# Kernel optimization log

Measured on AMD Instinct MI355X. Metric: run time of the kernel, lower is better.

Reference implementation:

```python
import jax, jax.numpy as jnp
import numpy as np

BN_EPS = 1e-5
EPS_GIN = 0.0  # pyg GINConv default eps

N_NODES = 50000
N_EDGES = 800000
D_IN = 128
D_OUT = 128


def setup_inputs() -> dict:
    key = jax.random.key(0)
    ks = jax.random.split(key, 6)
    x = jax.random.normal(ks[0], (N_NODES, D_IN), dtype=jnp.float32)
    edge_index = jax.random.randint(ks[1], (2, N_EDGES), 0, N_NODES, dtype=jnp.int32)
    # glorot-ish scale for the two Linear layers
    s1 = 1.0 / np.sqrt(D_IN)
    s2 = 1.0 / np.sqrt(D_OUT)
    W1 = jax.random.normal(ks[2], (D_IN, D_OUT), dtype=jnp.float32) * s1
    b1 = jnp.zeros((D_OUT,), dtype=jnp.float32)
    gamma = jnp.ones((D_OUT,), dtype=jnp.float32)
    beta = jnp.zeros((D_OUT,), dtype=jnp.float32)
    W2 = jax.random.normal(ks[3], (D_OUT, D_OUT), dtype=jnp.float32) * s2
    b2 = jnp.zeros((D_OUT,), dtype=jnp.float32)
    return {"x": x, "edge_index": edge_index, "W1": W1, "b1": b1,
            "gamma": gamma, "beta": beta, "W2": W2, "b2": b2}


def reference(x, edge_index, W1, b1, gamma, beta, W2, b2):
    n = x.shape[0]
    src, dst = edge_index[0], edge_index[1]  # source_to_target flow
    # scatter-add neighbor aggregation: agg[i] = sum_{(j->i)} x[j]
    agg = jax.ops.segment_sum(x[src], dst, num_segments=n)
    h = (1.0 + EPS_GIN) * x + agg  # GIN combine
    # Linear -> BatchNorm1d (training-mode batch stats, biased var) -> ReLU -> Linear
    h = h @ W1 + b1
    mean = jnp.mean(h, axis=0)
    var = jnp.var(h, axis=0)
    h = (h - mean) * jax.lax.rsqrt(var + BN_EPS) * gamma + beta
    h = jax.nn.relu(h)
    return h @ W2 + b2
```

## Files before the change

### kernel.cpp

```cpp
#include <hip/hip_runtime.h>
#include <hip/hip_bf16.h>

#define D 128
#define ELLW 64
#define BCAP 8192

typedef short bf16x8 __attribute__((ext_vector_type(8)));
typedef float f32x4 __attribute__((ext_vector_type(4)));

__device__ __forceinline__ ushort f32_to_bf16_rne(float f) {
    uint b = __float_as_uint(f);
    b += 0x7fffu + ((b >> 16) & 1u);
    return (ushort)(b >> 16);
}
__device__ __forceinline__ float bf16_bits_to_f32(ushort u) {
    return __uint_as_float(((uint)u) << 16);
}
__device__ __forceinline__ float blo(uint u) { return __uint_as_float(u << 16); }
__device__ __forceinline__ float bhi(uint u) { return __uint_as_float(u & 0xffff0000u); }


__global__ __launch_bounds__(512) void zero_kernel(int* __restrict__ p) {
    p[threadIdx.x] = 0;
}


__global__ __launch_bounds__(1024) void prep_scatter_kernel(const float2* __restrict__ x2,
                                                            const float* __restrict__ W1,
                                                            const float* __restrict__ W2,
                                                            const int* __restrict__ src,
                                                            const int* __restrict__ dst,
                                                            uint* __restrict__ xb,
                                                            ushort* __restrict__ W1T,
                                                            ushort* __restrict__ W2T,
                                                            uint* __restrict__ part,
                                                            int* __restrict__ bcnt,
                                                            int nhalf, int m, int nbx) {
    int b = blockIdx.x, t = threadIdx.x;
    if (b < nbx) {
        int i = b * 1024 + t;
        if (i < nhalf) {
            float2 v = x2[i];
            xb[i] = ((uint)f32_to_bf16_rne(v.y) << 16) | (uint)f32_to_bf16_rne(v.x);
        }
        return;
    }
    if (b < nbx + 32) {
        int wb = b - nbx;
        const float* W = (wb < 16) ? W1 : W2;
        ushort* WT = (wb < 16) ? W1T : W2T;
        int q = wb & 15;
        int nrow = q * 8 + (t >> 7);
        int k = t & 127;
        WT[nrow * D + k] = f32_to_bf16_rne(W[k * D + nrow]);
        return;
    }
    __shared__ int hist[256];
    __shared__ int cur[256];
    if (t < 256) hist[t] = 0;
    __syncthreads();

    int base = (b - nbx - 32) * 4096;
    uint v[4];
    int bk[4];
    bool ok[4];
#pragma unroll
    for (int j = 0; j < 4; ++j) {
        int e = base + j * 1024 + t;
        ok[j] = e < m;
        bk[j] = 0;
        if (ok[j]) {
            int s_ = src[e], d_ = dst[e];
            v[j] = ((uint)s_ << 16) | (uint)d_;
            bk[j] = d_ >> 8;
            atomicAdd(&hist[bk[j]], 1);
        }
    }
    __syncthreads();
    if (t < 256) {
        int h = hist[t];
        int g = h ? atomicAdd(&bcnt[t], h) : 0;
        cur[t] = t * BCAP + g;
    }
    __syncthreads();
#pragma unroll
    for (int j = 0; j < 4; ++j) {
        if (ok[j]) {
            int pos = atomicAdd(&cur[bk[j]], 1);
            if (pos - bk[j] * BCAP < BCAP)
                part[pos] = v[j];
        }
    }
}


__global__ __launch_bounds__(1024) void agg_gemm1_kernel(const uint* __restrict__ xb,
                                                         const uint* __restrict__ part,
                                                         const int* __restrict__ bcnt,
                                                         const ushort* __restrict__ W1T,
                                                         const float* __restrict__ bias,
                                                         ushort* __restrict__ h1b,
                                                         float* __restrict__ bn_sums,
                                                         int n) {
    __shared__ __align__(16) ushort hs[64 * D];
    __shared__ ushort lell[64 * ELLW];
    __shared__ int lcur[64];
    __shared__ float bs[D];
    __shared__ float bnl[2 * D];

    int tid = threadIdx.x;
    int row0 = blockIdx.x * 64;
    int bkt = row0 >> 8;
    if (tid < 64) lcur[tid] = 0;
    if (tid >= 128 && tid < 256) bs[tid - 128] = bias[tid - 128];
    if (tid >= 256 && tid < 512) bnl[tid - 256] = 0.f;
    __syncthreads();

    int cnt = min(bcnt[bkt], BCAP);
    const uint* pp = part + (size_t)bkt * BCAP;
    for (int i = tid; i < cnt; i += 1024) {
        uint v = pp[i];
        uint r2 = (v & 0xffffu) - (uint)row0;
        if (r2 < 64u) {
            int s = atomicAdd(&lcur[(int)r2], 1);
            s = min(s, ELLW - 1);
            lell[(int)r2 * ELLW + s] = (ushort)(v >> 16);
        }
    }
    __syncthreads();

    int w = tid >> 6, lane = tid & 63;
    char* hsb = (char*)hs;
    for (int i = 0; i < 4; ++i) {
        int r = w * 4 + i;
        int node = row0 + r;
        float sx = 0.f, sy = 0.f;
        if (node < n) {
            uint a = xb[node * 64 + lane];
            sx = blo(a);
            sy = bhi(a);
            int deg = min(lcur[r], ELLW);
            const ushort* lst = &lell[r * ELLW];
            int e = 0;
            for (; e + 7 < deg; e += 8) {
                uint u[8];
#pragma unroll
                for (int j = 0; j < 8; ++j) u[j] = xb[(int)lst[e + j] * 64 + lane];
#pragma unroll
                for (int j = 0; j < 8; ++j) { sx += blo(u[j]); sy += bhi(u[j]); }
            }
            if (e + 3 < deg) {
                uint u[4];
#pragma unroll
                for (int j = 0; j < 4; ++j) u[j] = xb[(int)lst[e + j] * 64 + lane];
#pragma unroll
                for (int j = 0; j < 4; ++j) { sx += blo(u[j]); sy += bhi(u[j]); }
                e += 4;
            }
            for (; e < deg; ++e) {
                uint u = xb[(int)lst[e] * 64 + lane];
                sx += blo(u);
                sy += bhi(u);
            }
        }
        uint o = ((uint)f32_to_bf16_rne(sy) << 16) | (uint)f32_to_bf16_rne(sx);
        *(uint*)(hsb + r * 256 + ((((lane >> 2) << 4) ^ ((r & 7) << 4)) | ((lane & 3) << 2))) = o;
    }
    __syncthreads();

    int band = w & 3, cq = w >> 2;
    int lrow = lane & 15, lk = lane >> 4;

    f32x4 acc[2];
#pragma unroll
    for (int f = 0; f < 2; ++f) acc[f] = (f32x4){0.f, 0.f, 0.f, 0.f};

    bf16x8 afr[4];
    int arow = band * 16 + lrow;
#pragma unroll
    for (int t = 0; t < 4; ++t)
        afr[t] = *(const bf16x8*)(hsb + arow * 256 + ((t * 64 + lk * 16) ^ ((arow & 7) << 4)));

#pragma unroll
    for (int f = 0; f < 2; ++f) {
        int nc = cq * 32 + f * 16 + lrow;
#pragma unroll
        for (int t = 0; t < 4; ++t) {
            bf16x8 bfr = *(const bf16x8*)(W1T + nc * D + t * 32 + lk * 8);
            acc[f] = __builtin_amdgcn_mfma_f32_16x16x32_bf16(afr[t], bfr, acc[f], 0, 0, 0);
        }
    }

    int rbase = row0 + band * 16 + lk * 4;
#pragma unroll
    for (int f = 0; f < 2; ++f) {
        int colc = cq * 32 + f * 16 + lrow;
        float bv = bs[colc];
        float s = 0.f, q = 0.f;
#pragma unroll
        for (int r = 0; r < 4; ++r) {
            int gr = rbase + r;
            if (gr < n) {
                float v = acc[f][r] + bv;
                h1b[(size_t)gr * D + colc] = f32_to_bf16_rne(v);
                s += v;
                q += v * v;
            }
        }
        s += __shfl_xor(s, 16, 64);
        s += __shfl_xor(s, 32, 64);
        q += __shfl_xor(q, 16, 64);
        q += __shfl_xor(q, 32, 64);
        if (lane < 16) {
            atomicAdd(&bnl[colc], s);
            atomicAdd(&bnl[D + colc], q);
        }
    }
    __syncthreads();
    if (tid < 2 * D) atomicAdd(&bn_sums[tid], bnl[tid]);
}


__global__ __launch_bounds__(256) void gemm2_kernel(const ushort* __restrict__ inb,
                                                    const ushort* __restrict__ WT,
                                                    const float* __restrict__ bias,
                                                    float* __restrict__ outp,
                                                    const float* __restrict__ gamma,
                                                    const float* __restrict__ beta,
                                                    const float* __restrict__ bn_sums,
                                                    float invn, int N) {
    __shared__ __align__(16) ushort hs[64 * D];
    __shared__ __align__(16) ushort wt[D * D];
    __shared__ float ss[2 * D];
    __shared__ float bs[D];

    int tid = threadIdx.x;
    int row0 = blockIdx.x * 64;
    if (tid < D) bs[tid] = bias[tid];
    if (tid < D) {
        float mean = bn_sums[tid] * invn;
        float var = bn_sums[D + tid] * invn - mean * mean;
        float sc = gamma[tid] * rsqrtf(var + 1e-5f);
        ss[tid] = sc;
        ss[D + tid] = beta[tid] - mean * sc;
    }
    __syncthreads();

    char* hsb = (char*)hs;
    char* wtb = (char*)wt;

#pragma unroll
    for (int it = 0; it < 8; ++it) {
        int c = it * 256 + tid;
        int wn = c >> 4, k8 = c & 15;
        bf16x8 v = *(const bf16x8*)(WT + wn * D + k8 * 8);
        *(bf16x8*)(wtb + wn * 256 + ((k8 * 16) ^ ((wn & 7) << 4))) = v;
    }
#pragma unroll
    for (int it = 0; it < 4; ++it) {
        int c = it * 256 + tid;
        int row = c >> 4, k8 = c & 15;
        int gr = row0 + row;
        bf16x8 v;
        if (gr < N) {
            v = *(const bf16x8*)(inb + (size_t)gr * D + k8 * 8);
        } else {
#pragma unroll
            for (int j = 0; j < 8; ++j) v[j] = 0;
        }
#pragma unroll
        for (int j = 0; j < 8; ++j) {
            int k = k8 * 8 + j;
            float f = bf16_bits_to_f32((ushort)v[j]);
            f = fmaxf(f * ss[k] + ss[D + k], 0.f);
            v[j] = (short)f32_to_bf16_rne(f);
        }
        *(bf16x8*)(hsb + row * 256 + ((k8 * 16) ^ ((row & 7) << 4))) = v;
    }
    __syncthreads();

    int w = tid >> 6, l = tid & 63;
    int lrow = l & 15, lk = l >> 4;

    f32x4 acc[8];
#pragma unroll
    for (int f = 0; f < 8; ++f) acc[f] = (f32x4){0.f, 0.f, 0.f, 0.f};

    bf16x8 afr[4];
    int arow = w * 16 + lrow;
#pragma unroll
    for (int t = 0; t < 4; ++t)
        afr[t] = *(const bf16x8*)(hsb + arow * 256 + ((t * 64 + lk * 16) ^ ((arow & 7) << 4)));

#pragma unroll
    for (int f = 0; f < 8; ++f) {
        int nc = f * 16 + lrow;
#pragma unroll
        for (int t = 0; t < 4; ++t) {
            bf16x8 bfr = *(const bf16x8*)(wtb + nc * 256 + ((t * 64 + lk * 16) ^ ((nc & 7) << 4)));
            acc[f] = __builtin_amdgcn_mfma_f32_16x16x32_bf16(afr[t], bfr, acc[f], 0, 0, 0);
        }
    }

    int rbase = row0 + w * 16 + lk * 4;
#pragma unroll
    for (int f = 0; f < 8; ++f) {
        int colc = f * 16 + lrow;
        float bv = bs[colc];
#pragma unroll
        for (int r = 0; r < 4; ++r) {
            int gr = rbase + r;
            if (gr < N) outp[(size_t)gr * D + colc] = acc[f][r] + bv;
        }
    }
}


extern "C" void kernel_launch(void* const* d_in, const int* in_sizes, int n_in,
                              void* d_out, int out_size, void* d_ws, size_t ws_size,
                              hipStream_t stream) {
    const float* x = (const float*)d_in[0];
    const int* edge = (const int*)d_in[1];
    const float* W1 = (const float*)d_in[2];
    const float* b1 = (const float*)d_in[3];
    const float* gamma = (const float*)d_in[4];
    const float* beta = (const float*)d_in[5];
    const float* W2 = (const float*)d_in[6];
    const float* b2 = (const float*)d_in[7];

    int n = in_sizes[0] / D;
    int m = in_sizes[1] / 2;
    const int* src = edge;
    const int* dst = edge + m;

    int nbuck = (n + 255) >> 8;

    uint* xb = (uint*)d_out;

    auto al = [](size_t o) { return (o + 63) & ~(size_t)63; };
    char* ws = (char*)d_ws;
    size_t off = 0;
    ushort* h1b = (ushort*)(ws + off); off = al(off + (size_t)n * D * sizeof(ushort));
    uint* part = (uint*)(ws + off);    off = al(off + (size_t)nbuck * BCAP * sizeof(uint));
    int* bcnt = (int*)(ws + off);      off += 256 * sizeof(int);
    float* bn_sums = (float*)(ws + off); off = al(off + 2 * D * sizeof(float));
    ushort* W1T = (ushort*)(ws + off); off = al(off + (size_t)D * D * sizeof(ushort));
    ushort* W2T = (ushort*)(ws + off); off = al(off + (size_t)D * D * sizeof(ushort));

    int nbx = (n * 64 + 1023) / 1024;
    int nbs = (m + 4095) / 4096;
    int nbg = (n + 63) / 64;

    zero_kernel<<<1, 512, 0, stream>>>(bcnt);
    prep_scatter_kernel<<<nbx + 32 + nbs, 1024, 0, stream>>>((const float2*)x, W1, W2, src, dst,
                                                             xb, W1T, W2T, part, bcnt, n * 64, m, nbx);
    agg_gemm1_kernel<<<nbg, 1024, 0, stream>>>(xb, part, bcnt, W1T, b1, h1b, bn_sums, n);
    gemm2_kernel<<<nbg, 256, 0, stream>>>(h1b, W2T, b2, (float*)d_out, gamma, beta,
                                          bn_sums, 1.0f / (float)n, n);
}
```

Measured before the change: 98.40 us.

## Fuse aggregation, GEMM1, BatchNorm and GEMM2 into persistent kernel with grid barrier

The separate agg_gemm1 and gemm2 kernels become one persistent kernel of 500 blocks, each handling up to two 64-row tiles. The GEMM1 accumulators stay in registers across a global atomic-counter barrier that waits for the BatchNorm sums to finish. After the barrier each block normalizes, applies ReLU and runs GEMM2 directly. This removes the bf16 h1 round trip through global memory and one kernel launch. The cost is a spin barrier that relies on all 500 blocks being co-resident, and fewer, more serialized blocks during the gather phase.

After: 382.8 us. 3.89x slower.

```diff
diff --git a/kernel.cpp b/kernel.cpp
--- a/kernel.cpp
+++ b/kernel.cpp
@@ -4,6 +4,7 @@
 #define D 128
 #define ELLW 64
 #define BCAP 8192
+#define GRID_FUSED 500
 
 typedef short bf16x8 __attribute__((ext_vector_type(8)));
 typedef float f32x4 __attribute__((ext_vector_type(4)));
@@ -13,14 +14,11 @@
     b += 0x7fffu + ((b >> 16) & 1u);
     return (ushort)(b >> 16);
 }
-__device__ __forceinline__ float bf16_bits_to_f32(ushort u) {
-    return __uint_as_float(((uint)u) << 16);
-}
 __device__ __forceinline__ float blo(uint u) { return __uint_as_float(u << 16); }
 __device__ __forceinline__ float bhi(uint u) { return __uint_as_float(u & 0xffff0000u); }
 
 
-__global__ __launch_bounds__(512) void zero_kernel(int* __restrict__ p) {
+__global__ __launch_bounds__(768) void zero_kernel(int* __restrict__ p) {
     p[threadIdx.x] = 0;
 }
 
@@ -94,223 +92,210 @@
 }
 
 
-__global__ __launch_bounds__(1024) void agg_gemm1_kernel(const uint* __restrict__ xb,
-                                                         const uint* __restrict__ part,
-                                                         const int* __restrict__ bcnt,
-                                                         const ushort* __restrict__ W1T,
-                                                         const float* __restrict__ bias,
-                                                         ushort* __restrict__ h1b,
-                                                         float* __restrict__ bn_sums,
-                                                         int n) {
+__global__ __launch_bounds__(1024, 8) void agg_mlp_kernel(const uint* __restrict__ xb,
+                                                          const uint* __restrict__ part,
+                                                          const int* __restrict__ bcnt,
+                                                          const ushort* __restrict__ W1T,
+                                                          const ushort* __restrict__ W2T,
+                                                          const float* __restrict__ b1,
+                                                          const float* __restrict__ b2,
+                                                          const float* __restrict__ gamma,
+                                                          const float* __restrict__ beta,
+                                                          float* __restrict__ bn_sums,
+                                                          int* __restrict__ counter,
+                                                          float* __restrict__ outp,
+                                                          float invn, int n, int nbg) {
     __shared__ __align__(16) ushort hs[64 * D];
     __shared__ ushort lell[64 * ELLW];
     __shared__ int lcur[64];
-    __shared__ float bs[D];
+    __shared__ float bs1[D], bs2[D];
     __shared__ float bnl[2 * D];
+    __shared__ float ss[2 * D];
 
     int tid = threadIdx.x;
-    int row0 = blockIdx.x * 64;
-    int bkt = row0 >> 8;
-    if (tid < 64) lcur[tid] = 0;
-    if (tid >= 128 && tid < 256) bs[tid - 128] = bias[tid - 128];
-    if (tid >= 256 && tid < 512) bnl[tid - 256] = 0.f;
-    __syncthreads();
-
-    int cnt = min(bcnt[bkt], BCAP);
-    const uint* pp = part + (size_t)bkt * BCAP;
-    for (int i = tid; i < cnt; i += 1024) {
-        uint v = pp[i];
-        uint r2 = (v & 0xffffu) - (uint)row0;
-        if (r2 < 64u) {
-            int s = atomicAdd(&lcur[(int)r2], 1);
-            s = min(s, ELLW - 1);
-            lell[(int)r2 * ELLW + s] = (ushort)(v >> 16);
-        }
-    }
-    __syncthreads();
-
     int w = tid >> 6, lane = tid & 63;
-    char* hsb = (char*)hs;
-    for (int i = 0; i < 4; ++i) {
-        int r = w * 4 + i;
-        int node = row0 + r;
-        float sx = 0.f, sy = 0.f;
-        if (node < n) {
-            uint a = xb[node * 64 + lane];
-            sx = blo(a);
-            sy = bhi(a);
-            int deg = min(lcur[r], ELLW);
-            const ushort* lst = &lell[r * ELLW];
-            int e = 0;
-            for (; e + 7 < deg; e += 8) {
-                uint u[8];
-#pragma unroll
-                for (int j = 0; j < 8; ++j) u[j] = xb[(int)lst[e + j] * 64 + lane];
-#pragma unroll
-                for (int j = 0; j < 8; ++j) { sx += blo(u[j]); sy += bhi(u[j]); }
-            }
-            if (e + 3 < deg) {
-                uint u[4];
-#pragma unroll
-                for (int j = 0; j < 4; ++j) u[j] = xb[(int)lst[e + j] * 64 + lane];
-#pragma unroll
-                for (int j = 0; j < 4; ++j) { sx += blo(u[j]); sy += bhi(u[j]); }
-                e += 4;
-            }
-            for (; e < deg; ++e) {
-                uint u = xb[(int)lst[e] * 64 + lane];
-                sx += blo(u);
-                sy += bhi(u);
-            }
-        }
-        uint o = ((uint)f32_to_bf16_rne(sy) << 16) | (uint)f32_to_bf16_rne(sx);
-        *(uint*)(hsb + r * 256 + ((((lane >> 2) << 4) ^ ((r & 7) << 4)) | ((lane & 3) << 2))) = o;
-    }
-    __syncthreads();
-
     int band = w & 3, cq = w >> 2;
     int lrow = lane & 15, lk = lane >> 4;
-
-    f32x4 acc[2];
-#pragma unroll
-    for (int f = 0; f < 2; ++f) acc[f] = (f32x4){0.f, 0.f, 0.f, 0.f};
-
-    bf16x8 afr[4];
-    int arow = band * 16 + lrow;
-#pragma unroll
-    for (int t = 0; t < 4; ++t)
-        afr[t] = *(const bf16x8*)(hsb + arow * 256 + ((t * 64 + lk * 16) ^ ((arow & 7) << 4)));
-
-#pragma unroll
-    for (int f = 0; f < 2; ++f) {
-        int nc = cq * 32 + f * 16 + lrow;
-#pragma unroll
-        for (int t = 0; t < 4; ++t) {
-            bf16x8 bfr = *(const bf16x8*)(W1T + nc * D + t * 32 + lk * 8);
-            acc[f] = __builtin_amdgcn_mfma_f32_16x16x32_bf16(afr[t], bfr, acc[f], 0, 0, 0);
-        }
-    }
-
-    int rbase = row0 + band * 16 + lk * 4;
-#pragma unroll
-    for (int f = 0; f < 2; ++f) {
-        int colc = cq * 32 + f * 16 + lrow;
-        float bv = bs[colc];
-        float s = 0.f, q = 0.f;
-#pragma unroll
-        for (int r = 0; r < 4; ++r) {
-            int gr = rbase + r;
-            if (gr < n) {
-                float v = acc[f][r] + bv;
-                h1b[(size_t)gr * D + colc] = f32_to_bf16_rne(v);
-                s += v;
-                q += v * v;
-            }
-        }
-        s += __shfl_xor(s, 16, 64);
-        s += __shfl_xor(s, 32, 64);
-        q += __shfl_xor(q, 16, 64);
-        q += __shfl_xor(q, 32, 64);
-        if (lane < 16) {
-            atomicAdd(&bnl[colc], s);
-            atomicAdd(&bnl[D + colc], q);
-        }
-    }
+    char* hsb = (char*)hs;
+
+    if (tid < D) bs1[tid] = b1[tid];
+    else if (tid < 2 * D) bs2[tid - D] = b2[tid - D];
+    if (tid >= 512 && tid < 768) bnl[tid - 512] = 0.f;
+
+    f32x4 acc[2][2];
+#pragma unroll
+    for (int s = 0; s < 2; ++s)
+#pragma unroll
+        for (int f = 0; f < 2; ++f) acc[s][f] = (f32x4){0.f, 0.f, 0.f, 0.f};
+
+#pragma unroll
+    for (int s = 0; s < 2; ++s) {
+        int tile = blockIdx.x + s * GRID_FUSED;
+        if (tile < nbg) {
+            int row0 = tile * 64;
+            int bkt = row0 >> 8;
+            __syncthreads();
+            if (tid < 64) lcur[tid] = 0;
+            __syncthreads();
+            int cnt = min(bcnt[bkt], BCAP);
+            const uint* pp = part + (size_t)bkt * BCAP;
+            for (int i = tid; i < cnt; i += 1024) {
+                uint v = pp[i];
+                uint r2 = (v & 0xffffu) - (uint)row0;
+                if (r2 < 64u) {
+                    int sl = atomicAdd(&lcur[(int)r2], 1);
+                    sl = min(sl, ELLW - 1);
+                    lell[(int)r2 * ELLW + sl] = (ushort)(v >> 16);
+                }
+            }
+            __syncthreads();
+            for (int i = 0; i < 4; ++i) {
+                int r = w * 4 + i;
+                int node = row0 + r;
+                float sx = 0.f, sy = 0.f;
+                if (node < n) {
+                    uint a = xb[node * 64 + lane];
+                    sx = blo(a);
+                    sy = bhi(a);
+                    int deg = min(lcur[r], ELLW);
+                    const ushort* lst = &lell[r * ELLW];
+                    int e = 0;
+                    for (; e + 7 < deg; e += 8) {
+                        uint u[8];
+#pragma unroll
+                        for (int j = 0; j < 8; ++j) u[j] = xb[(int)lst[e + j] * 64 + lane];
+#pragma unroll
+                        for (int j = 0; j < 8; ++j) { sx += blo(u[j]); sy += bhi(u[j]); }
+                    }
+                    if (e + 3 < deg) {
+                        uint u[4];
+#pragma unroll
+                        for (int j = 0; j < 4; ++j) u[j] = xb[(int)lst[e + j] * 64 + lane];
+#pragma unroll
+                        for (int j = 0; j < 4; ++j) { sx += blo(u[j]); sy += bhi(u[j]); }
+                        e += 4;
+                    }
+                    for (; e < deg; ++e) {
+                        uint u = xb[(int)lst[e] * 64 + lane];
+                        sx += blo(u);
+                        sy += bhi(u);
+                    }
+                }
+                uint o = ((uint)f32_to_bf16_rne(sy) << 16) | (uint)f32_to_bf16_rne(sx);
+                *(uint*)(hsb + r * 256 +
+                         ((((lane >> 2) << 4) ^ ((r & 7) << 4)) | ((lane & 3) << 2))) = o;
+            }
+            __syncthreads();
+            bf16x8 afr[4];
+            int arow = band * 16 + lrow;
+#pragma unroll
+            for (int t = 0; t < 4; ++t)
+                afr[t] = *(const bf16x8*)(hsb + arow * 256 +
+                                          ((t * 64 + lk * 16) ^ ((arow & 7) << 4)));
+#pragma unroll
+            for (int f = 0; f < 2; ++f) {
+                int nc = cq * 32 + f * 16 + lrow;
+#pragma unroll
+                for (int t = 0; t < 4; ++t) {
+                    bf16x8 bfr = *(const bf16x8*)(W1T + nc * D + t * 32 + lk * 8);
+                    acc[s][f] = __builtin_amdgcn_mfma_f32_16x16x32_bf16(afr[t], bfr, acc[s][f], 0, 0, 0);
+                }
+            }
+            int rbase = row0 + band * 16 + lk * 4;
+#pragma unroll
+            for (int f = 0; f < 2; ++f) {
+                int colc = cq * 32 + f * 16 + lrow;
+                float bv = bs1[colc];
+                float s1 = 0.f, q1 = 0.f;
+#pragma unroll
+                for (int r = 0; r < 4; ++r) {
+                    float v = acc[s][f][r] + bv;
+                    acc[s][f][r] = v;
+                    int gr = rbase + r;
+                    if (gr < n) { s1 += v; q1 += v * v; }
+                }
+                s1 += __shfl_xor(s1, 16, 64);
+                s1 += __shfl_xor(s1, 32, 64);
+                q1 += __shfl_xor(q1, 16, 64);
+                q1 += __shfl_xor(q1, 32, 64);
+                if (lane < 16) {
+                    atomicAdd(&bnl[colc], s1);
+                    atomicAdd(&bnl[D + colc], q1);
+                }
+            }
+        }
+    }
+
     __syncthreads();
     if (tid < 2 * D) atomicAdd(&bn_sums[tid], bnl[tid]);
-}
-
-
-__global__ __launch_bounds__(256) void gemm2_kernel(const ushort* __restrict__ inb,
-                                                    const ushort* __restrict__ WT,
-                                                    const float* __restrict__ bias,
-                                                    float* __restrict__ outp,
-                                                    const float* __restrict__ gamma,
-                                                    const float* __restrict__ beta,
-                                                    const float* __restrict__ bn_sums,
-                                                    float invn, int N) {
-    __shared__ __align__(16) ushort hs[64 * D];
-    __shared__ __align__(16) ushort wt[D * D];
-    __shared__ float ss[2 * D];
-    __shared__ float bs[D];
-
-    int tid = threadIdx.x;
-    int row0 = blockIdx.x * 64;
-    if (tid < D) bs[tid] = bias[tid];
+    __threadfence();
+    __syncthreads();
+    if (tid == 0) {
+        atomicAdd(counter, 1);
+        while (atomicAdd(counter, 0) < GRID_FUSED) __builtin_amdgcn_s_sleep(2);
+    }
+    __syncthreads();
+    __threadfence();
+
+    if (tid < 2 * D) ss[tid] = atomicAdd(&bn_sums[tid], 0.0f);
+    __syncthreads();
     if (tid < D) {
-        float mean = bn_sums[tid] * invn;
-        float var = bn_sums[D + tid] * invn - mean * mean;
+        float mean = ss[tid] * invn;
+        float var = ss[D + tid] * invn - mean * mean;
         float sc = gamma[tid] * rsqrtf(var + 1e-5f);
         ss[tid] = sc;
         ss[D + tid] = beta[tid] - mean * sc;
     }
     __syncthreads();
 
-    char* hsb = (char*)hs;
-    char* wtb = (char*)wt;
-
-#pragma unroll
-    for (int it = 0; it < 8; ++it) {
-        int c = it * 256 + tid;
-        int wn = c >> 4, k8 = c & 15;
-        bf16x8 v = *(const bf16x8*)(WT + wn * D + k8 * 8);
-        *(bf16x8*)(wtb + wn * 256 + ((k8 * 16) ^ ((wn & 7) << 4))) = v;
-    }
-#pragma unroll
-    for (int it = 0; it < 4; ++it) {
-        int c = it * 256 + tid;
-        int row = c >> 4, k8 = c & 15;
-        int gr = row0 + row;
-        bf16x8 v;
-        if (gr < N) {
-            v = *(const bf16x8*)(inb + (size_t)gr * D + k8 * 8);
-        } else {
-#pragma unroll
-            for (int j = 0; j < 8; ++j) v[j] = 0;
-        }
-#pragma unroll
-        for (int j = 0; j < 8; ++j) {
-            int k = k8 * 8 + j;
-            float f = bf16_bits_to_f32((ushort)v[j]);
-            f = fmaxf(f * ss[k] + ss[D + k], 0.f);
-            v[j] = (short)f32_to_bf16_rne(f);
-        }
-        *(bf16x8*)(hsb + row * 256 + ((k8 * 16) ^ ((row & 7) << 4))) = v;
-    }
-    __syncthreads();
-
-    int w = tid >> 6, l = tid & 63;
-    int lrow = l & 15, lk = l >> 4;
-
-    f32x4 acc[8];
-#pragma unroll
-    for (int f = 0; f < 8; ++f) acc[f] = (f32x4){0.f, 0.f, 0.f, 0.f};
-
-    bf16x8 afr[4];
-    int arow = w * 16 + lrow;
-#pragma unroll
-    for (int t = 0; t < 4; ++t)
-        afr[t] = *(const bf16x8*)(hsb + arow * 256 + ((t * 64 + lk * 16) ^ ((arow & 7) << 4)));
-
-#pragma unroll
-    for (int f = 0; f < 8; ++f) {
-        int nc = f * 16 + lrow;
-#pragma unroll
-        for (int t = 0; t < 4; ++t) {
-            bf16x8 bfr = *(const bf16x8*)(wtb + nc * 256 + ((t * 64 + lk * 16) ^ ((nc & 7) << 4)));
-            acc[f] = __builtin_amdgcn_mfma_f32_16x16x32_bf16(afr[t], bfr, acc[f], 0, 0, 0);
-        }
-    }
-
-    int rbase = row0 + w * 16 + lk * 4;
-#pragma unroll
-    for (int f = 0; f < 8; ++f) {
-        int colc = f * 16 + lrow;
-        float bv = bs[colc];
-#pragma unroll
-        for (int r = 0; r < 4; ++r) {
-            int gr = rbase + r;
-            if (gr < N) outp[(size_t)gr * D + colc] = acc[f][r] + bv;
+#pragma unroll
+    for (int s = 0; s < 2; ++s) {
+        int tile = blockIdx.x + s * GRID_FUSED;
+        if (tile < nbg) {
+            int row0 = tile * 64;
+            __syncthreads();
+            int rbl = band * 16 + lk * 4;
+#pragma unroll
+            for (int f = 0; f < 2; ++f) {
+                int colc = cq * 32 + f * 16 + lrow;
+                float sc = ss[colc], sh = ss[D + colc];
+#pragma unroll
+                for (int r = 0; r < 4; ++r) {
+                    float v = fmaxf(acc[s][f][r] * sc + sh, 0.f);
+                    int rl = rbl + r;
+                    *(ushort*)(hsb + rl * 256 + ((colc * 2) ^ ((rl & 7) << 4))) = f32_to_bf16_rne(v);
+                }
+            }
+            __syncthreads();
+            bf16x8 afr[4];
+            int arow = band * 16 + lrow;
+#pragma unroll
+            for (int t = 0; t < 4; ++t)
+                afr[t] = *(const bf16x8*)(hsb + arow * 256 +
+                                          ((t * 64 + lk * 16) ^ ((arow & 7) << 4)));
+            f32x4 a2[2];
+#pragma unroll
+            for (int f = 0; f < 2; ++f) a2[f] = (f32x4){0.f, 0.f, 0.f, 0.f};
+#pragma unroll
+            for (int f = 0; f < 2; ++f) {
+                int nc = cq * 32 + f * 16 + lrow;
+#pragma unroll
+                for (int t = 0; t < 4; ++t) {
+                    bf16x8 bfr = *(const bf16x8*)(W2T + nc * D + t * 32 + lk * 8);
+                    a2[f] = __builtin_amdgcn_mfma_f32_16x16x32_bf16(afr[t], bfr, a2[f], 0, 0, 0);
+                }
+            }
+            int rbase = row0 + band * 16 + lk * 4;
+#pragma unroll
+            for (int f = 0; f < 2; ++f) {
+                int colc = cq * 32 + f * 16 + lrow;
+                float bv = bs2[colc];
+#pragma unroll
+                for (int r = 0; r < 4; ++r) {
+                    int gr = rbase + r;
+                    if (gr < n) outp[(size_t)gr * D + colc] = a2[f][r] + bv;
+                }
+            }
         }
     }
 }
@@ -340,10 +325,11 @@
     auto al = [](size_t o) { return (o + 63) & ~(size_t)63; };
     char* ws = (char*)d_ws;
     size_t off = 0;
-    ushort* h1b = (ushort*)(ws + off); off = al(off + (size_t)n * D * sizeof(ushort));
     uint* part = (uint*)(ws + off);    off = al(off + (size_t)nbuck * BCAP * sizeof(uint));
-    int* bcnt = (int*)(ws + off);      off += 256 * sizeof(int);
-    float* bn_sums = (float*)(ws + off); off = al(off + 2 * D * sizeof(float));
+    int* bcnt = (int*)(ws + off);      off += 768 * sizeof(int);
+    float* bn_sums = (float*)(bcnt + 256);
+    int* counter = bcnt + 512;
+    off = al(off);
     ushort* W1T = (ushort*)(ws + off); off = al(off + (size_t)D * D * sizeof(ushort));
     ushort* W2T = (ushort*)(ws + off); off = al(off + (size_t)D * D * sizeof(ushort));
 
@@ -351,10 +337,10 @@
     int nbs = (m + 4095) / 4096;
     int nbg = (n + 63) / 64;
 
-    zero_kernel<<<1, 512, 0, stream>>>(bcnt);
+    zero_kernel<<<1, 768, 0, stream>>>(bcnt);
     prep_scatter_kernel<<<nbx + 32 + nbs, 1024, 0, stream>>>((const float2*)x, W1, W2, src, dst,
                                                              xb, W1T, W2T, part, bcnt, n * 64, m, nbx);
-    agg_gemm1_kernel<<<nbg, 1024, 0, stream>>>(xb, part, bcnt, W1T, b1, h1b, bn_sums, n);
-    gemm2_kernel<<<nbg, 256, 0, stream>>>(h1b, W2T, b2, (float*)d_out, gamma, beta,
-                                          bn_sums, 1.0f / (float)n, n);
-}
+    agg_mlp_kernel<<<GRID_FUSED, 1024, 0, stream>>>(xb, part, bcnt, W1T, W2T, b1, b2, gamma, beta,
+                                                    bn_sums, counter, (float*)d_out,
+                                                    1.0f / (float)n, n, nbg);
+}
```
